# Kernel tuning notes

Hardware: AMD Instinct MI355X
Metric: run time of the kernel (lower is better)

Reference implementation:

```python
import jax, jax.numpy as jnp
import numpy as np

WEIGHT = 1000.0      # start/end cell penalty
LONELY_W = 15.0      # cell lit outside cluster
CLUSTER_W = 5.0      # cell unlit inside cluster
CELL_W = 20.0        # cell on a shortest manhattan path
CSIZE_W = 12.0       # cluster-size penalty
GAP_W = 300.0        # gap-to-endpoint penalty
H = W = 10


def _md(y1, x1, y2, x2):
    return jnp.abs(y1 - y2) + jnp.abs(x1 - x2)


def _per_sample(result, points):
    # result: [H, W] float, points: [2, 2] int (row, col) of start and end
    p0y, p0x = points[0, 0], points[0, 1]
    p1y, p1x = points[1, 0], points[1, 1]
    base = _md(p0y, p0x, p1y, p1x)

    loss_start = (2.0 - (result[p0y, p0x] + result[p1y, p1x])) * WEIGHT

    # 8-connected flood fill from start over cells whose value rounds to 1.
    mask = jnp.round(result) == 1.0
    seed = jnp.zeros((H, W), bool).at[p0y, p0x].set(True)

    def dilate(_, c):
        p = jnp.pad(c, 1)
        nb = (p[:-2, :-2] | p[:-2, 1:-1] | p[:-2, 2:] |
              p[1:-1, :-2] | p[1:-1, 2:] |
              p[2:, :-2] | p[2:, 1:-1] | p[2:, 2:])
        return c | (nb & mask)

    # 8-connected diameter of a 10x10 grid is 9; H+W iterations is a safe bound.
    cluster = jax.lax.fori_loop(0, H + W, dilate, seed)

    rows = jnp.arange(H)[:, None]
    cols = jnp.arange(W)[None, :]

    # per-cell manhattan detour penalty
    d2 = _md(rows, cols, p0y, p0x) + _md(rows, cols, p1y, p1x)
    delta = (d2 - base).astype(result.dtype)
    single_cell = jnp.sum(jnp.where(delta == 0.0,
                                    (1.0 - result) * CELL_W,
                                    result * delta * 0.5))

    # NB: the original tests [column, row] membership against [row, col]
    # cluster entries -> transposed membership map. Faithfully reproduced.
    in_cl = cluster.T
    csize = jnp.sum(cluster).astype(result.dtype)
    lonelyness = jnp.sum(jnp.where(in_cl, (1.0 - result) * CLUSTER_W,
                                   result * LONELY_W))
    cluster_size_pen = jnp.sum(jnp.where(in_cl, result * csize * CSIZE_W, 0.0))

    # nearest cluster cell to the end point (strict improvement over base)
    dist_end = _md(rows, cols, p1y, p1x)
    masked = jnp.where(cluster, dist_end, H * W + 10).reshape(-1)
    idx = jnp.argmin(masked)
    minval = masked[idx]
    better = minval < base
    ny = jnp.where(better, idx // W, p0y)
    nx = jnp.where(better, idx % W, p0x)
    gap = jnp.minimum(base, minval)

    oy = p1y - ny
    ox = p1x - nx

    def upd(cond, cy, cx, st):
        by, bx, bg = st
        d = _md(cy, cx, p1y, p1x)
        b = cond & (d < bg)
        return (jnp.where(b, cy, by), jnp.where(b, cx, bx), jnp.where(b, d, bg))

    st = (ny, nx, gap)
    c = ox < 0
    st = upd(c, ny, nx - 1, st)
    st = upd(c & (ny != 0), ny - 1, nx - 1, st)
    st = upd(c & (ny != H - 1), ny + 1, nx - 1, st)
    c = ox > 0
    st = upd(c, ny, nx + 1, st)
    st = upd(c & (ny != 0), ny - 1, nx + 1, st)
    st = upd(c & (ny != H - 1), ny + 1, nx + 1, st)
    st = upd(oy < 0, ny - 1, nx, st)
    st = upd(oy > 0, ny + 1, nx, st)
    ncy = jnp.clip(st[0], 0, H - 1)
    ncx = jnp.clip(st[1], 0, W - 1)

    gap_pen = gap.astype(result.dtype) * GAP_W * (1.0 - result[ncy, ncx])

    return loss_start + lonelyness + single_cell + cluster_size_pen + gap_pen


def setup_inputs() -> dict:
    key = jax.random.key(0)
    k1, k2 = jax.random.split(key)
    B = 262144
    result_given = jax.random.uniform(k1, (B, 1, H, W), dtype=jnp.float32)
    points_given = jax.random.randint(k2, (B, 2, 2), 0, 10, dtype=jnp.int64 if jax.config.jax_enable_x64 else jnp.int32)
    return {"result_given": result_given, "points_given": points_given}


def reference(result_given, points_given):
    losses = jax.vmap(_per_sample)(result_given[:, 0], points_given)
    return jnp.sum(losses).reshape(1)
```

## Files before the change

### kernel.cpp

```cpp
#include <hip/hip_runtime.h>
#include <cstdint>

#define GH 10
#define GW 10

__global__ __launch_bounds__(256, 4) void custom_loss_kernel(
    const float* __restrict__ result,
    const int* __restrict__ points,
    float* __restrict__ out,
    int B)
{
    const int tid = blockIdx.x * blockDim.x + threadIdx.x;
    const int s = tid >> 2;
    const int q = tid & 3;
    float loss = 0.f;
    if (s < B) {
        const float* __restrict__ r = result + (size_t)s * 100;
        const int4 p = ((const int4*)points)[s];
        const int p0y = p.x, p0x = p.y, p1y = p.z, p1x = p.w;
        const int dy0 = abs(p0y - p1y), dx0 = abs(p0x - p1x);
        const int base0 = dy0 + dx0;
        const int idx0 = p0y * GW + p0x;
        const int idx1 = p1y * GW + p1x;
        const float rs = r[idx0];
        const float re = r[idx1];
        const float p0yf = (float)p0y, p0xf = (float)p0x;
        const float p1yf = (float)p1y, p1xf = (float)p1x;
        const float dy0f = (float)dy0, dx0f = (float)dx0;
        const float basef = (float)base0;

        float4 v4[7];
#pragma unroll
        for (int i = 0; i < 6; ++i) v4[i] = ((const float4*)r)[4 * i + q];
        v4[6] = make_float4(0.f, 0.f, 0.f, 0.f);
        if (q == 0) v4[6] = ((const float4*)r)[24];

        float sum_p = 0.f, scA = 0.f, scB = 0.f, box_p = 0.f;
        uint64_t mlo = 0, mhi = 0;
#pragma unroll
        for (int i = 0; i < 7; ++i) {
            const int kbase = (i < 6) ? 4 * (4 * i + q) : (96 + 4 * q);
            const int y0 = (kbase * 205) >> 11;
            const int x0 = kbase - 10 * y0;
            const float y0f = (float)y0, x0f = (float)x0;
            const float sy0 = fabsf(y0f - p0yf) + fabsf(y0f - p1yf);
            const float sy1 = fabsf(y0f + 1.f - p0yf) + fabsf(y0f + 1.f - p1yf);
            const bool wrap = (x0 == 8);
            const float vv[4] = {v4[i].x, v4[i].y, v4[i].z, v4[i].w};
            uint32_t nib = 0;
#pragma unroll
            for (int j = 0; j < 4; ++j) {
                const bool w = wrap && (j >= 2);
                const float xf = x0f + (w ? (float)(j - 10) : (float)j);
                const float syj = w ? sy1 : sy0;
                const float v = vv[j];
                const float sx = fabsf(xf - p0xf) + fabsf(xf - p1xf);
                sum_p += v;
                scA = fmaf(syj, v, scA);
                scB = fmaf(sx, v, scB);
                box_p += ((sx == dx0f) & (syj == dy0f)) ? v : 0.f;
                nib |= (v > 0.5f) ? (1u << j) : 0u;
            }
            const uint64_t n64 = (uint64_t)nib;
            const int shhi = (kbase >= 50) ? (kbase - 50) : 0;
            mlo |= (kbase <= 44) ? (n64 << kbase)
                                 : ((kbase == 48) ? ((n64 & 3ull) << 48) : 0);
            mhi |= (kbase >= 52) ? (n64 << shhi)
                                 : ((kbase == 48) ? (n64 >> 2) : 0);
        }
        sum_p += __shfl_xor(sum_p, 1); sum_p += __shfl_xor(sum_p, 2);
        scA   += __shfl_xor(scA, 1);   scA   += __shfl_xor(scA, 2);
        scB   += __shfl_xor(scB, 1);   scB   += __shfl_xor(scB, 2);
        box_p += __shfl_xor(box_p, 1); box_p += __shfl_xor(box_p, 2);
        mlo |= (uint64_t)__shfl_xor((unsigned long long)mlo, 1);
        mlo |= (uint64_t)__shfl_xor((unsigned long long)mlo, 2);
        mhi |= (uint64_t)__shfl_xor((unsigned long long)mhi, 1);
        mhi |= (uint64_t)__shfl_xor((unsigned long long)mhi, 2);
        const float sum_all = sum_p, boxSum = box_p;
        const float sc = fmaf(-basef, sum_all, scA + scB);

        const uint64_t M50 = (1ull << 50) - 1;
        const uint64_t C0  = 0x10040100401ull;
        const uint64_t NC0 = M50 & ~C0;
        const uint64_t NC9 = M50 & ~(C0 << 9);
        const int half = q >> 1;
        const uint64_t mw = half ? mhi : mlo;
        uint64_t c = 0;
        if (half == 0 && idx0 < 50)  c = 1ull << idx0;
        if (half == 1 && idx0 >= 50) c = 1ull << (idx0 - 50);
#pragma unroll 1
        for (int it = 0; it < GH + GW; ++it) {
            const uint64_t ho = c | ((c << 1) & NC0) | ((c >> 1) & NC9);
            const uint64_t hoth = (uint64_t)__shfl_xor((unsigned long long)ho, 2);
            const uint64_t inc = half ? (hoth >> 40) : ((hoth & 0x3FFull) << 40);
            const uint64_t n = ((ho | (ho << 10) | (ho >> 10) | inc) & mw) | c;
            int ch = (n != c) ? 1 : 0;
            ch += __shfl_xor(ch, 2);
            c = n;
            if (!ch) break;
        }
        int Kh = __popcll(c);
        const int K = Kh + __shfl_xor(Kh, 2);
        const uint64_t coth = (uint64_t)__shfl_xor((unsigned long long)c, 2);
        const uint64_t clo = half ? coth : c;
        const uint64_t chi = half ? c : coth;
        const uint32_t cl32 = (uint32_t)clo;

        float st_p = 0.f;
#pragma unroll
        for (int i = 0; i < 7; ++i) {
            const int kbase = (i < 6) ? 4 * (4 * i + q) : (96 + 4 * q);
            const int y0 = (kbase * 205) >> 11;
            const int x0 = kbase - 10 * y0;
            const int s0 = x0 * 10 + y0;
            const uint64_t tA = (clo >> (s0 & 63)) | (chi << ((50 - s0) & 63));
            const uint64_t tB = chi >> ((s0 - 50) & 63);
            const uint32_t tl = (uint32_t)((s0 < 50) ? tA : tB);
            uint32_t nib = (tl & 1u) | ((tl >> 9) & 2u) |
                           ((tl >> 18) & 4u) | ((tl >> 27) & 8u);
            if (x0 == 8) {
                const uint32_t b2 = (cl32 >> (y0 + 1)) & 1u;
                const uint32_t b3 = (cl32 >> (y0 + 11)) & 1u;
                nib = (nib & 3u) | (b2 << 2) | (b3 << 3);
            }
            const float vv[4] = {v4[i].x, v4[i].y, v4[i].z, v4[i].w};
#pragma unroll
            for (int j = 0; j < 4; ++j)
                st_p += (nib & (1u << j)) ? vv[j] : 0.f;
        }
        st_p += __shfl_xor(st_p, 1); st_p += __shfl_xor(st_p, 2);
        const float S_T = st_p;

        int bestkey = 0x7FFFFFFF;
#pragma unroll
        for (int k = 0; k < 3; ++k) {
            const int y = q + 4 * k;
            if (y < GH) {
                const uint32_t rb = (uint32_t)(((y < 5) ? (clo >> (10 * y))
                                                        : (chi >> (10 * (y - 5)))) & 0x3FFull);
                const uint32_t left  = rb & ((2u << p1x) - 1);
                const uint32_t right = rb >> p1x;
                const int dl = left  ? (p1x - (31 - __builtin_clz(left))) : 1000;
                const int dr = right ? __builtin_ctz(right) : 1000;
                int dx, xx;
                if (dl <= dr) { dx = dl; xx = p1x - dl; }
                else          { dx = dr; xx = p1x + dr; }
                const int key = ((abs(y - p1y) + dx) << 7) | (y * GW + xx);
                if (rb && key < bestkey) bestkey = key;
            }
        }
        bestkey = min(bestkey, __shfl_xor(bestkey, 1));
        bestkey = min(bestkey, __shfl_xor(bestkey, 2));
        const int bestd = bestkey >> 7;
        const int bidx = bestkey & 127;

        const bool better = bestd < base0;
        const int ny = better ? bidx / 10 : p0y;
        const int nx = better ? bidx % 10 : p0x;
        const int gap = min(base0, bestd);

        int by = ny, bx = nx, bg = gap;
        const int oy = p1y - ny, ox = p1x - nx;
        auto upd = [&](bool cond, int cy, int cx) {
            const int d = abs(cy - p1y) + abs(cx - p1x);
            if (cond && (d < bg)) { by = cy; bx = cx; bg = d; }
        };
        upd(ox < 0,                     ny,     nx - 1);
        upd((ox < 0) && (ny != 0),      ny - 1, nx - 1);
        upd((ox < 0) && (ny != GH - 1), ny + 1, nx - 1);
        upd(ox > 0,                     ny,     nx + 1);
        upd((ox > 0) && (ny != 0),      ny - 1, nx + 1);
        upd((ox > 0) && (ny != GH - 1), ny + 1, nx + 1);
        upd(oy < 0,                     ny - 1, nx);
        upd(oy > 0,                     ny + 1, nx);
        const int ncy = min(max(by, 0), GH - 1);
        const int ncx = min(max(bx, 0), GW - 1);
        const float rn = r[ncy * GW + ncx];

        const float csf = (float)K;
        const float nboxf = (float)((dy0 + 1) * (dx0 + 1));
        const float loss_start = (2.f - (rs + re)) * 1000.f;
        const float lon = 5.f * csf + 15.f * sum_all - 20.f * S_T;
        const float single_cell = 0.5f * sc + 20.f * (nboxf - boxSum);
        const float cpen = 12.f * csf * S_T;
        const float gap_pen = (float)gap * 300.f * (1.f - rn);
        loss = loss_start + lon + single_cell + cpen + gap_pen;
        if (q != 0) loss = 0.f;
    }

#pragma unroll
    for (int off = 32; off > 0; off >>= 1)
        loss += __shfl_down(loss, off);
    __shared__ float wsum[4];
    const int lane = threadIdx.x & 63;
    const int wid = threadIdx.x >> 6;
    if (lane == 0) wsum[wid] = loss;
    __syncthreads();
    if (threadIdx.x == 0)
        atomicAdd(out, wsum[0] + wsum[1] + wsum[2] + wsum[3]);
}

extern "C" void kernel_launch(void* const* d_in, const int* in_sizes, int n_in,
                              void* d_out, int out_size, void* d_ws, size_t ws_size,
                              hipStream_t stream)
{
    const float* result = (const float*)d_in[0];
    const int* points   = (const int*)d_in[1];
    float* out = (float*)d_out;
    const int B = in_sizes[0] / 100;
    hipMemsetAsync(out, 0, sizeof(float), stream);
    const int block = 256;
    const int grid = (4 * B + block - 1) / block;
    custom_loss_kernel<<<grid, block, 0, stream>>>(result, points, out, B);
}
```

Before: 185.3 us.

## Run flood fill and endpoint search single-threaded per sample via shared memory

After: 188.7 us. No clear change (+1.8%).

```diff
diff --git a/kernel.cpp b/kernel.cpp
--- a/kernel.cpp
+++ b/kernel.cpp
@@ -4,32 +4,41 @@
 #define GH 10
 #define GW 10
 
-__global__ __launch_bounds__(256, 4) void custom_loss_kernel(
+__global__ __launch_bounds__(256, 6) void custom_loss_kernel(
     const float* __restrict__ result,
     const int* __restrict__ points,
     float* __restrict__ out,
     int B)
 {
-    const int tid = blockIdx.x * blockDim.x + threadIdx.x;
-    const int s = tid >> 2;
-    const int q = tid & 3;
-    float loss = 0.f;
-    if (s < B) {
-        const float* __restrict__ r = result + (size_t)s * 100;
-        const int4 p = ((const int4*)points)[s];
+    __shared__ uint64_t sMlo[64], sMhi[64];
+    __shared__ uint64_t sClo[64], sChi[64];
+    __shared__ float    sGapPen[64];
+    __shared__ int      sK[64];
+    __shared__ float    wsum[4];
+
+    const int tix = threadIdx.x;
+    const int s_local = tix >> 2;
+    const int q = tix & 3;
+    const int gs = blockIdx.x * 64 + s_local;
+    const bool valid = (gs < B);
+
+    float4 v4[7];
+    float sum_all = 0.f, sc = 0.f, boxSum = 0.f, rs = 0.f, re = 0.f;
+    int dy0i = 0, dx0i = 0;
+    if (valid) {
+        const float* __restrict__ r = result + (size_t)gs * 100;
+        const int4 p = ((const int4*)points)[gs];
         const int p0y = p.x, p0x = p.y, p1y = p.z, p1x = p.w;
-        const int dy0 = abs(p0y - p1y), dx0 = abs(p0x - p1x);
-        const int base0 = dy0 + dx0;
+        dy0i = abs(p0y - p1y); dx0i = abs(p0x - p1x);
+        const float dy0f = (float)dy0i, dx0f = (float)dx0i;
+        const float basef = dy0f + dx0f;
         const int idx0 = p0y * GW + p0x;
         const int idx1 = p1y * GW + p1x;
-        const float rs = r[idx0];
-        const float re = r[idx1];
+        rs = r[idx0];
+        re = r[idx1];
         const float p0yf = (float)p0y, p0xf = (float)p0x;
         const float p1yf = (float)p1y, p1xf = (float)p1x;
-        const float dy0f = (float)dy0, dx0f = (float)dx0;
-        const float basef = (float)base0;
-
-        float4 v4[7];
+
 #pragma unroll
         for (int i = 0; i < 6; ++i) v4[i] = ((const float4*)r)[4 * i + q];
         v4[6] = make_float4(0.f, 0.f, 0.f, 0.f);
@@ -76,36 +85,88 @@
         mlo |= (uint64_t)__shfl_xor((unsigned long long)mlo, 2);
         mhi |= (uint64_t)__shfl_xor((unsigned long long)mhi, 1);
         mhi |= (uint64_t)__shfl_xor((unsigned long long)mhi, 2);
-        const float sum_all = sum_p, boxSum = box_p;
-        const float sc = fmaf(-basef, sum_all, scA + scB);
-
-        const uint64_t M50 = (1ull << 50) - 1;
-        const uint64_t C0  = 0x10040100401ull;
-        const uint64_t NC0 = M50 & ~C0;
-        const uint64_t NC9 = M50 & ~(C0 << 9);
-        const int half = q >> 1;
-        const uint64_t mw = half ? mhi : mlo;
-        uint64_t c = 0;
-        if (half == 0 && idx0 < 50)  c = 1ull << idx0;
-        if (half == 1 && idx0 >= 50) c = 1ull << (idx0 - 50);
+        sum_all = sum_p; boxSum = box_p;
+        sc = fmaf(-basef, sum_p, scA + scB);
+        if (q == 0) { sMlo[s_local] = mlo; sMhi[s_local] = mhi; }
+    }
+    __syncthreads();
+
+    if (tix < 64) {
+        const int fgs = blockIdx.x * 64 + tix;
+        if (fgs < B) {
+            const int4 p = ((const int4*)points)[fgs];
+            const int p0y = p.x, p0x = p.y, p1y = p.z, p1x = p.w;
+            const int base0 = abs(p0y - p1y) + abs(p0x - p1x);
+            const int idx0 = p0y * GW + p0x;
+            const uint64_t mlo = sMlo[tix], mhi = sMhi[tix];
+
+            const uint64_t M50 = (1ull << 50) - 1;
+            const uint64_t C0  = 0x10040100401ull;
+            const uint64_t NC0 = M50 & ~C0;
+            const uint64_t NC9 = M50 & ~(C0 << 9);
+            uint64_t clo = 0, chi = 0;
+            if (idx0 < 50) clo = 1ull << idx0; else chi = 1ull << (idx0 - 50);
 #pragma unroll 1
-        for (int it = 0; it < GH + GW; ++it) {
-            const uint64_t ho = c | ((c << 1) & NC0) | ((c >> 1) & NC9);
-            const uint64_t hoth = (uint64_t)__shfl_xor((unsigned long long)ho, 2);
-            const uint64_t inc = half ? (hoth >> 40) : ((hoth & 0x3FFull) << 40);
-            const uint64_t n = ((ho | (ho << 10) | (ho >> 10) | inc) & mw) | c;
-            int ch = (n != c) ? 1 : 0;
-            ch += __shfl_xor(ch, 2);
-            c = n;
-            if (!ch) break;
-        }
-        int Kh = __popcll(c);
-        const int K = Kh + __shfl_xor(Kh, 2);
-        const uint64_t coth = (uint64_t)__shfl_xor((unsigned long long)c, 2);
-        const uint64_t clo = half ? coth : c;
-        const uint64_t chi = half ? c : coth;
+            for (int it = 0; it < GH + GW; ++it) {
+                const uint64_t hlo = clo | ((clo << 1) & NC0) | ((clo >> 1) & NC9);
+                const uint64_t hhi = chi | ((chi << 1) & NC0) | ((chi >> 1) & NC9);
+                uint64_t nlo = (hlo | (hlo << 10) | (hlo >> 10) | ((hhi & 0x3FFull) << 40)) & mlo;
+                uint64_t nhi = (hhi | (hhi << 10) | (hhi >> 10) | (hlo >> 40)) & mhi;
+                nlo |= clo; nhi |= chi;
+                if (nlo == clo && nhi == chi) break;
+                clo = nlo; chi = nhi;
+            }
+            const int K = __popcll(clo) + __popcll(chi);
+
+            int bestd = 1000, bidx = 0;
+#pragma unroll
+            for (int y = 0; y < GH; ++y) {
+                const uint32_t rb = (uint32_t)(((y < 5) ? (clo >> (10 * y))
+                                                        : (chi >> (10 * (y - 5)))) & 0x3FFull);
+                const uint32_t left  = rb & ((2u << p1x) - 1);
+                const uint32_t right = rb >> p1x;
+                const int dl = left  ? (p1x - (31 - __builtin_clz(left))) : 1000;
+                const int dr = right ? __builtin_ctz(right) : 1000;
+                int dx, xx;
+                if (dl <= dr) { dx = dl; xx = p1x - dl; }
+                else          { dx = dr; xx = p1x + dr; }
+                const int d = abs(y - p1y) + dx;
+                if (rb && d < bestd) { bestd = d; bidx = y * GW + xx; }
+            }
+
+            const bool better = bestd < base0;
+            const int ny = better ? bidx / 10 : p0y;
+            const int nx = better ? bidx % 10 : p0x;
+            const int gap = min(base0, bestd);
+
+            int by = ny, bx = nx, bg = gap;
+            const int oy = p1y - ny, ox = p1x - nx;
+            auto upd = [&](bool cond, int cy, int cx) {
+                const int d = abs(cy - p1y) + abs(cx - p1x);
+                if (cond && (d < bg)) { by = cy; bx = cx; bg = d; }
+            };
+            upd(ox < 0,                     ny,     nx - 1);
+            upd((ox < 0) && (ny != 0),      ny - 1, nx - 1);
+            upd((ox < 0) && (ny != GH - 1), ny + 1, nx - 1);
+            upd(ox > 0,                     ny,     nx + 1);
+            upd((ox > 0) && (ny != 0),      ny - 1, nx + 1);
+            upd((ox > 0) && (ny != GH - 1), ny + 1, nx + 1);
+            upd(oy < 0,                     ny - 1, nx);
+            upd(oy > 0,                     ny + 1, nx);
+            const int ncy = min(max(by, 0), GH - 1);
+            const int ncx = min(max(bx, 0), GW - 1);
+            const float rn = result[(size_t)fgs * 100 + ncy * GW + ncx];
+
+            sClo[tix] = clo; sChi[tix] = chi; sK[tix] = K;
+            sGapPen[tix] = (float)gap * 300.f * (1.f - rn);
+        }
+    }
+    __syncthreads();
+
+    float loss = 0.f;
+    if (valid) {
+        const uint64_t clo = sClo[s_local], chi = sChi[s_local];
         const uint32_t cl32 = (uint32_t)clo;
-
         float st_p = 0.f;
 #pragma unroll
         for (int i = 0; i < 7; ++i) {
@@ -129,69 +190,21 @@
                 st_p += (nib & (1u << j)) ? vv[j] : 0.f;
         }
         st_p += __shfl_xor(st_p, 1); st_p += __shfl_xor(st_p, 2);
-        const float S_T = st_p;
-
-        int bestkey = 0x7FFFFFFF;
-#pragma unroll
-        for (int k = 0; k < 3; ++k) {
-            const int y = q + 4 * k;
-            if (y < GH) {
-                const uint32_t rb = (uint32_t)(((y < 5) ? (clo >> (10 * y))
-                                                        : (chi >> (10 * (y - 5)))) & 0x3FFull);
-                const uint32_t left  = rb & ((2u << p1x) - 1);
-                const uint32_t right = rb >> p1x;
-                const int dl = left  ? (p1x - (31 - __builtin_clz(left))) : 1000;
-                const int dr = right ? __builtin_ctz(right) : 1000;
-                int dx, xx;
-                if (dl <= dr) { dx = dl; xx = p1x - dl; }
-                else          { dx = dr; xx = p1x + dr; }
-                const int key = ((abs(y - p1y) + dx) << 7) | (y * GW + xx);
-                if (rb && key < bestkey) bestkey = key;
-            }
-        }
-        bestkey = min(bestkey, __shfl_xor(bestkey, 1));
-        bestkey = min(bestkey, __shfl_xor(bestkey, 2));
-        const int bestd = bestkey >> 7;
-        const int bidx = bestkey & 127;
-
-        const bool better = bestd < base0;
-        const int ny = better ? bidx / 10 : p0y;
-        const int nx = better ? bidx % 10 : p0x;
-        const int gap = min(base0, bestd);
-
-        int by = ny, bx = nx, bg = gap;
-        const int oy = p1y - ny, ox = p1x - nx;
-        auto upd = [&](bool cond, int cy, int cx) {
-            const int d = abs(cy - p1y) + abs(cx - p1x);
-            if (cond && (d < bg)) { by = cy; bx = cx; bg = d; }
-        };
-        upd(ox < 0,                     ny,     nx - 1);
-        upd((ox < 0) && (ny != 0),      ny - 1, nx - 1);
-        upd((ox < 0) && (ny != GH - 1), ny + 1, nx - 1);
-        upd(ox > 0,                     ny,     nx + 1);
-        upd((ox > 0) && (ny != 0),      ny - 1, nx + 1);
-        upd((ox > 0) && (ny != GH - 1), ny + 1, nx + 1);
-        upd(oy < 0,                     ny - 1, nx);
-        upd(oy > 0,                     ny + 1, nx);
-        const int ncy = min(max(by, 0), GH - 1);
-        const int ncx = min(max(bx, 0), GW - 1);
-        const float rn = r[ncy * GW + ncx];
-
-        const float csf = (float)K;
-        const float nboxf = (float)((dy0 + 1) * (dx0 + 1));
-        const float loss_start = (2.f - (rs + re)) * 1000.f;
-        const float lon = 5.f * csf + 15.f * sum_all - 20.f * S_T;
-        const float single_cell = 0.5f * sc + 20.f * (nboxf - boxSum);
-        const float cpen = 12.f * csf * S_T;
-        const float gap_pen = (float)gap * 300.f * (1.f - rn);
-        loss = loss_start + lon + single_cell + cpen + gap_pen;
-        if (q != 0) loss = 0.f;
+
+        if (q == 0) {
+            const float csf = (float)sK[s_local];
+            const float nboxf = (float)((dy0i + 1) * (dx0i + 1));
+            const float loss_start = (2.f - (rs + re)) * 1000.f;
+            const float lon = 5.f * csf + 15.f * sum_all - 20.f * st_p;
+            const float single_cell = 0.5f * sc + 20.f * (nboxf - boxSum);
+            const float cpen = 12.f * csf * st_p;
+            loss = loss_start + lon + single_cell + cpen + sGapPen[s_local];
+        }
     }
 
 #pragma unroll
     for (int off = 32; off > 0; off >>= 1)
         loss += __shfl_down(loss, off);
-    __shared__ float wsum[4];
     const int lane = threadIdx.x & 63;
     const int wid = threadIdx.x >> 6;
     if (lane == 0) wsum[wid] = loss;
@@ -210,6 +223,6 @@
     const int B = in_sizes[0] / 100;
     hipMemsetAsync(out, 0, sizeof(float), stream);
     const int block = 256;
-    const int grid = (4 * B + block - 1) / block;
+    const int grid = (B + 63) / 64;
     custom_loss_kernel<<<grid, block, 0, stream>>>(result, points, out, B);
 }
```
